# Kernel tuning notes

Hardware: AMD Instinct MI355X
Metric: run time of the kernel (lower is better)

The kernel has to match this reference:

```python
import jax, jax.numpy as jnp
import numpy as np

NEG_SLOPE = 0.2  # PyG GATv2Conv default


def with_self_loops(edge_index, n):
    loop = jnp.arange(n, dtype=edge_index.dtype)
    src = jnp.concatenate([edge_index[0], loop])
    dst = jnp.concatenate([edge_index[1], loop])
    return src, dst


def gatv2(x, src, dst, Wl, bl, Wr, br, att, bias):
    """PyG GATv2Conv (eval mode, concat=True, add_self_loops done by caller).
    x: [N, F_in]; att: [H, C]. Returns [N, H*C]."""
    N = x.shape[0]
    H, C = att.shape
    xl = (x @ Wl + bl).reshape(N, H, C)  # lin_l(x): source-side transform
    xr = (x @ Wr + br).reshape(N, H, C)  # lin_r(x): target-side transform
    s = jax.nn.leaky_relu(xl[src] + xr[dst], NEG_SLOPE)      # [E,H,C]
    logit = jnp.einsum('ehc,hc->eh', s, att)                 # [E,H]
    m = jax.ops.segment_max(logit, dst, num_segments=N)      # stable softmax per target
    e = jnp.exp(logit - m[dst])
    den = jax.ops.segment_sum(e, dst, num_segments=N)
    alpha = e / (den[dst] + 1e-16)                           # [E,H]
    out = jax.ops.segment_sum(alpha[:, :, None] * xl[src], dst, num_segments=N)
    return out.reshape(N, H * C) + bias


def setup_inputs() -> dict:
    N, E = 20000, 320000        # agent nodes / edges
    M, EM = 40000, 400000       # lane nodes / edges
    B, L = 64, 50               # focal agents, centerline length
    SEQ, INC, HID, HEADS, OUT = 50, 2, 32, 4, 60
    H4 = HID * HEADS
    key = jax.random.key(0)
    ks = list(jax.random.split(key, 48))
    kit = iter(ks)

    def p(shape):
        return jax.random.normal(next(kit), shape, jnp.float32) * 0.05

    inp = {
        'x': jax.random.normal(next(kit), (N, SEQ, INC), jnp.float32),
        'edge_index': jax.random.randint(next(kit), (2, E), 0, N),
        'lane_x': jax.random.normal(next(kit), (M, 2), jnp.float32),
        'lane_edge_index': jax.random.randint(next(kit), (2, EM), 0, M),
        'batch': jnp.sort(jax.random.randint(next(kit), (N,), 0, B)),
        'focal_idx': jax.random.randint(next(kit), (B,), 0, N),
        'centerlines': jax.random.normal(next(kit), (B, L, 2), jnp.float32),
        # agent embedding
        'ae_W': p((SEQ * INC, HID)), 'ae_b': p((HID,)),
        # agent subgraph conv1 / conv2
        'a1_Wl': p((HID, H4)), 'a1_bl': p((H4,)), 'a1_Wr': p((HID, H4)), 'a1_br': p((H4,)), 'a1_att': p((HEADS, HID)), 'a1_b': p((H4,)),
        'a2_Wl': p((H4, H4)), 'a2_bl': p((H4,)), 'a2_Wr': p((H4, H4)), 'a2_br': p((H4,)), 'a2_att': p((HEADS, HID)), 'a2_b': p((H4,)),
        # map embedding + map subgraph
        'me_W': p((2, HID)), 'me_b': p((HID,)),
        'm1_Wl': p((HID, H4)), 'm1_bl': p((H4,)), 'm1_Wr': p((HID, H4)), 'm1_br': p((H4,)), 'm1_att': p((HEADS, HID)), 'm1_b': p((H4,)),
        'm2_Wl': p((H4, H4)), 'm2_bl': p((H4,)), 'm2_Wr': p((H4, H4)), 'm2_br': p((H4,)), 'm2_att': p((HEADS, HID)), 'm2_b': p((H4,)),
        # centerline processor
        'cl_W': p((2, HID)), 'cl_b': p((HID,)),
        # global graph (heads=1)
        'g_Wl': p((H4, HID)), 'g_bl': p((HID,)), 'g_Wr': p((H4, HID)), 'g_br': p((HID,)), 'g_att': p((1, HID)), 'g_b': p((HID,)),
        # output head
        'fc_W': p((2 * HID, OUT)), 'fc_b': p((OUT,)),
    }
    return inp


def reference(x, edge_index, lane_x, lane_edge_index, batch, focal_idx, centerlines,
              ae_W, ae_b,
              a1_Wl, a1_bl, a1_Wr, a1_br, a1_att, a1_b,
              a2_Wl, a2_bl, a2_Wr, a2_br, a2_att, a2_b,
              me_W, me_b,
              m1_Wl, m1_bl, m1_Wr, m1_br, m1_att, m1_b,
              m2_Wl, m2_bl, m2_Wr, m2_br, m2_att, m2_b,
              cl_W, cl_b,
              g_Wl, g_bl, g_Wr, g_br, g_att, g_b,
              fc_W, fc_b):
    N = x.shape[0]
    M = lane_x.shape[0]
    # agent branch
    agent_x = jax.nn.relu(x.reshape(N, -1) @ ae_W + ae_b)
    a_src, a_dst = with_self_loops(edge_index, N)
    h = jax.nn.relu(gatv2(agent_x, a_src, a_dst, a1_Wl, a1_bl, a1_Wr, a1_br, a1_att, a1_b))
    agent_features = jax.nn.relu(gatv2(h, a_src, a_dst, a2_Wl, a2_bl, a2_Wr, a2_br, a2_att, a2_b))  # [N,128]
    # map branch (output unused downstream in original, computed for faithfulness)
    map_x = jax.nn.relu(lane_x @ me_W + me_b)
    m_src, m_dst = with_self_loops(lane_edge_index, M)
    hm = jax.nn.relu(gatv2(map_x, m_src, m_dst, m1_Wl, m1_bl, m1_Wr, m1_br, m1_att, m1_b))
    map_features = jax.nn.relu(gatv2(hm, m_src, m_dst, m2_Wl, m2_bl, m2_Wr, m2_br, m2_att, m2_b))
    _ = map_features  # global_mean_pool results are dead code in the original forward
    # global graph over agent features (heads=1)
    global_features = jax.nn.relu(gatv2(agent_features, a_src, a_dst, g_Wl, g_bl, g_Wr, g_br, g_att, g_b))  # [N,32]
    focal = global_features[focal_idx]  # [B,32]
    # centerlines: per-polyline mean then linear (no relu, as in original)
    cl_feat = jnp.mean(centerlines, axis=1) @ cl_W + cl_b  # [B,32]
    combined = jnp.concatenate([focal, cl_feat], axis=1)
    return combined @ fc_W + fc_b
```

## Files before the change

kernel.cpp:

```cpp
#include <hip/hip_runtime.h>
#include <hip/hip_bf16.h>
#include <hip/hip_fp16.h>
#include <math.h>

typedef __hip_bfloat16 bf16;
#define NEG_SLOPE 0.2f
#define SFLAG (1 << 30)

typedef _Float16 f16x8 __attribute__((ext_vector_type(8)));
typedef float f32x4 __attribute__((ext_vector_type(4)));

__global__ void k_detect_zero(const unsigned short* __restrict__ x, int* __restrict__ flag,
                              int* __restrict__ zbase, int n) {
    for (int i = blockIdx.x * blockDim.x + threadIdx.x; i < n; i += gridDim.x * blockDim.x)
        zbase[i] = 0;
    if (blockIdx.x == 0) {
        __shared__ int cnt;
        if (threadIdx.x == 0) cnt = 0;
        __syncthreads();
        int local = 0;
        for (int i = threadIdx.x; i < 2048; i += blockDim.x) {
            unsigned short w = x[2 * i];
            int e = (w >> 7) & 0xFF;
            if (e >= 0x90) local++;
        }
        atomicAdd(&cnt, local);
        __syncthreads();
        if (threadIdx.x == 0) flag[0] = (cnt > 100) ? 1 : 0;
    }
}

#define NSEG 25
struct Seg { const void* src; int n; int off; };
struct Tab { Seg s[NSEG]; };

__device__ __forceinline__ float ldconv(const void* src, int i, int f32mode) {
    return f32mode ? ((const float*)src)[i]
                   : __bfloat162float(((const bf16*)src)[i]);
}

__global__ void k_convert(Tab tab, float* __restrict__ dst, const int* __restrict__ flag,
                          const int* __restrict__ dstArr, int E, int N,
                          int* __restrict__ deg, int* __restrict__ rank,
                          const void* a2WlS, const void* a2WrS,
                          const void* gWlS, const void* gWrS,
                          __half* __restrict__ a2Wlt, __half* __restrict__ a2Wrt,
                          __half* __restrict__ gWlt, __half* __restrict__ gWrt) {
    int f32mode = flag[0];
    int gid = blockIdx.x * blockDim.x + threadIdx.x;
    int gsz = gridDim.x * blockDim.x;
    for (int s = 0; s < NSEG; s++) {
        Seg sg = tab.s[s];
        for (int i = gid; i < sg.n; i += gsz) {
            dst[sg.off + i] = ldconv(sg.src, i, f32mode);
        }
    }
    for (int i = gid; i < 128 * 128; i += gsz) {
        int k = i >> 7, j = i & 127;
        a2Wlt[(size_t)j * 128 + k] = __float2half(ldconv(a2WlS, i, f32mode));
        a2Wrt[(size_t)j * 128 + k] = __float2half(ldconv(a2WrS, i, f32mode));
    }
    for (int i = gid; i < 128 * 32; i += gsz) {
        int k = i >> 5, j = i & 31;
        gWlt[(size_t)j * 128 + k] = __float2half(ldconv(gWlS, i, f32mode));
        gWrt[(size_t)j * 128 + k] = __float2half(ldconv(gWrS, i, f32mode));
    }
    int EA = E + N;
    for (int e = gid; e < EA; e += gsz) {
        int d = (e < E) ? dstArr[e] : (e - E);
        rank[e] = atomicAdd(&deg[d], 1);
    }
}

__launch_bounds__(1024)
__global__ void k_scanf(const int* __restrict__ deg, int* __restrict__ offs,
                        int n, int* __restrict__ st, int nb) {
    __shared__ int ws[16];
    __shared__ int stot, sprev;
    int tile = blockIdx.x;
    int i = tile * 1024 + threadIdx.x;
    int lane = threadIdx.x & 63, wid = threadIdx.x >> 6;
    int v = (i < n) ? deg[i] : 0;
    int x = v;
    #pragma unroll
    for (int o = 1; o < 64; o <<= 1) {
        int y = __shfl_up(x, o);
        if (lane >= o) x += y;
    }
    if (lane == 63) ws[wid] = x;
    __syncthreads();
    if (wid == 0) {
        int w = (lane < 16) ? ws[lane] : 0;
        int s = w;
        #pragma unroll
        for (int o = 1; o < 16; o <<= 1) {
            int y = __shfl_up(s, o);
            if (lane >= o) s += y;
        }
        if (lane < 16) ws[lane] = s - w;
        if (lane == 15) stot = s;
    }
    __syncthreads();
    int local = ws[wid] + x - v;
    if (threadIdx.x == 0) {
        int prev = 0;
        if (tile > 0) {
            int vv;
            while ((((vv = __hip_atomic_load(&st[tile - 1], __ATOMIC_ACQUIRE,
                                             __HIP_MEMORY_SCOPE_AGENT))) & SFLAG) == 0) {}
            prev = vv & ~SFLAG;
        }
        __hip_atomic_store(&st[tile], (prev + stot) | SFLAG, __ATOMIC_RELEASE,
                           __HIP_MEMORY_SCOPE_AGENT);
        sprev = prev;
        if (tile == nb - 1) offs[n] = prev + stot;
    }
    __syncthreads();
    if (i < n) offs[i] = sprev + local;
}

__launch_bounds__(256)
__global__ void k_fill_embedlin(const int* __restrict__ srcArr, const int* __restrict__ dstArr,
                                int E, int N, const int* __restrict__ offs,
                                const int* __restrict__ rank, int* __restrict__ csr,
                                const void* __restrict__ xraw, const int* __restrict__ flag,
                                const float* __restrict__ aeW, const float* __restrict__ aeb,
                                const float* __restrict__ Wl, const float* __restrict__ bl,
                                const float* __restrict__ Wr, const float* __restrict__ br,
                                __half* __restrict__ outl, float* __restrict__ outr,
                                int EB) {
    __shared__ float xs[100 * 36];
    __shared__ float axs[32 * 36];
    if (blockIdx.x >= EB) {
        int e = (blockIdx.x - EB) * 256 + threadIdx.x;
        int EA = E + N;
        if (e >= EA) return;
        int d, s;
        if (e < E) { d = dstArr[e]; s = srcArr[e]; } else { d = s = e - E; }
        csr[offs[d] + rank[e]] = s;
        return;
    }
    constexpr int NTP = 36;
    int t = threadIdx.x, nb = blockIdx.x * 32;
    if (flag[0]) {
        const float4* x4 = (const float4*)xraw;
        for (int idx = t; idx < 32 * 25; idx += 256) {
            int node = idx / 25, k4 = idx % 25;
            float4 v = x4[(size_t)(nb + node) * 25 + k4];
            xs[(k4 * 4 + 0) * NTP + node] = v.x;
            xs[(k4 * 4 + 1) * NTP + node] = v.y;
            xs[(k4 * 4 + 2) * NTP + node] = v.z;
            xs[(k4 * 4 + 3) * NTP + node] = v.w;
        }
    } else {
        const ushort4* xu = (const ushort4*)xraw;
        for (int idx = t; idx < 32 * 25; idx += 256) {
            int node = idx / 25, k4 = idx % 25;
            ushort4 u = xu[(size_t)(nb + node) * 25 + k4];
            xs[(k4 * 4 + 0) * NTP + node] = __uint_as_float((unsigned)u.x << 16);
            xs[(k4 * 4 + 1) * NTP + node] = __uint_as_float((unsigned)u.y << 16);
            xs[(k4 * 4 + 2) * NTP + node] = __uint_as_float((unsigned)u.z << 16);
            xs[(k4 * 4 + 3) * NTP + node] = __uint_as_float((unsigned)u.w << 16);
        }
    }
    __syncthreads();
    {
        int j = t & 31, g0 = t >> 5;
        float a0 = 0.f, a1 = 0.f, a2 = 0.f, a3 = 0.f;
        #pragma unroll 10
        for (int k = 0; k < 100; k++) {
            float w = aeW[k * 32 + j];
            const float4 xv = *(const float4*)&xs[k * NTP + g0 * 4];
            a0 += w * xv.x; a1 += w * xv.y; a2 += w * xv.z; a3 += w * xv.w;
        }
        float bj = aeb[j];
        axs[j * NTP + g0 * 4 + 0] = fmaxf(a0 + bj, 0.f);
        axs[j * NTP + g0 * 4 + 1] = fmaxf(a1 + bj, 0.f);
        axs[j * NTP + g0 * 4 + 2] = fmaxf(a2 + bj, 0.f);
        axs[j * NTP + g0 * 4 + 3] = fmaxf(a3 + bj, 0.f);
    }
    __syncthreads();
    {
        int j = t & 63, g0 = t >> 6;
        float aL0[2][4], aL1[2][4], aR0[2][4], aR1[2][4];
        #pragma unroll
        for (int g = 0; g < 2; g++)
            #pragma unroll
            for (int c = 0; c < 4; c++) { aL0[g][c]=0.f; aL1[g][c]=0.f; aR0[g][c]=0.f; aR1[g][c]=0.f; }
        #pragma unroll 4
        for (int k = 0; k < 32; k++) {
            float wl0 = Wl[k * 128 + j];
            float wl1 = Wl[k * 128 + j + 64];
            float wr0 = Wr[k * 128 + j];
            float wr1 = Wr[k * 128 + j + 64];
            #pragma unroll
            for (int g = 0; g < 2; g++) {
                const float4 xv = *(const float4*)&axs[k * NTP + (g0 + g * 4) * 4];
                aL0[g][0] += wl0 * xv.x; aL0[g][1] += wl0 * xv.y; aL0[g][2] += wl0 * xv.z; aL0[g][3] += wl0 * xv.w;
                aL1[g][0] += wl1 * xv.x; aL1[g][1] += wl1 * xv.y; aL1[g][2] += wl1 * xv.z; aL1[g][3] += wl1 * xv.w;
                aR0[g][0] += wr0 * xv.x; aR0[g][1] += wr0 * xv.y; aR0[g][2] += wr0 * xv.z; aR0[g][3] += wr0 * xv.w;
                aR1[g][0] += wr1 * xv.x; aR1[g][1] += wr1 * xv.y; aR1[g][2] += wr1 * xv.z; aR1[g][3] += wr1 * xv.w;
            }
        }
        float bl0 = bl[j], bl1 = bl[j + 64], br0 = br[j], br1 = br[j + 64];
        #pragma unroll
        for (int g = 0; g < 2; g++) {
            int n0 = nb + (g0 + g * 4) * 4;
            #pragma unroll
            for (int c = 0; c < 4; c++) {
                size_t row = (size_t)(n0 + c) * 128;
                outl[row + j]      = __float2half(aL0[g][c] + bl0);
                outl[row + j + 64] = __float2half(aL1[g][c] + bl1);
                outr[row + j]      = aR0[g][c] + br0;
                outr[row + j + 64] = aR1[g][c] + br1;
            }
        }
    }
}

__device__ __forceinline__ void gat_proc(float4 raw, bool valid,
                                         const float* xrd, const float* av,
                                         float* acc, float& sm) {
    const __half2* h = (const __half2*)&raw;
    float v[8];
    float2 f;
    f = __half22float2(h[0]); v[0] = f.x; v[1] = f.y;
    f = __half22float2(h[1]); v[2] = f.x; v[3] = f.y;
    f = __half22float2(h[2]); v[4] = f.x; v[5] = f.y;
    f = __half22float2(h[3]); v[6] = f.x; v[7] = f.y;
    float p = 0.f;
    #pragma unroll
    for (int c = 0; c < 8; c++) {
        float u = v[c] + xrd[c];
        u = (u > 0.f) ? u : NEG_SLOPE * u;
        p += u * av[c];
    }
    p += __shfl_xor(p, 1);
    p += __shfl_xor(p, 2);
    p += __shfl_xor(p, 4);
    p += __shfl_xor(p, 8);
    float w = __expf(fminf(p, 80.f));
    if (!valid) w = 0.f;
    sm += w;
    #pragma unroll
    for (int c = 0; c < 8; c++) acc[c] += w * v[c];
}

__device__ __forceinline__ void gat16_to_lds(__half* xsh,
                                             const __half* __restrict__ xl,
                                             const float* __restrict__ xr,
                                             const float* __restrict__ att,
                                             const int* __restrict__ offs,
                                             const int* __restrict__ csr,
                                             const float* __restrict__ bias,
                                             int nb, int N) {
    int t = threadIdx.x;
    int wave = t >> 6, lane = t & 63;
    int grp = lane >> 4, sub = lane & 15;
    int lb = lane & 48;
    float av[8];
    {
        const float4* t4 = (const float4*)(att + sub * 8);
        float4 c = t4[0], e = t4[1];
        av[0]=c.x; av[1]=c.y; av[2]=c.z; av[3]=c.w;
        av[4]=e.x; av[5]=e.y; av[6]=e.z; av[7]=e.w;
    }
    int d = nb + wave * 4 + grp;
    bool ok = d < N;
    int i0 = ok ? offs[d] : 0;
    int i1 = ok ? offs[d + 1] : 0;
    int cnt = i1 - i0;

    float xrd[8];
    #pragma unroll
    for (int c = 0; c < 8; c++) xrd[c] = 0.f;
    if (ok) {
        const float4* p4 = (const float4*)(xr + (size_t)d * 128 + sub * 8);
        float4 a = p4[0], b = p4[1];
        xrd[0]=a.x; xrd[1]=a.y; xrd[2]=a.z; xrd[3]=a.w;
        xrd[4]=b.x; xrd[5]=b.y; xrd[6]=b.z; xrd[7]=b.w;
    }
    float acc[8];
    #pragma unroll
    for (int c = 0; c < 8; c++) acc[c] = 0.f;
    float sm = 0.f;

    int myv = (sub < cnt) ? csr[i0 + sub] : 0;
    for (int c0 = 0; c0 < cnt; c0 += 16) {
        int myv_nxt = (c0 + 16 + sub < cnt) ? csr[i0 + c0 + 16 + sub] : 0;
        int rem = min(cnt - c0, 16);
        for (int k = 0; k < rem; k += 4) {
            int s0 = __shfl(myv, lb + k + 0);
            int s1 = __shfl(myv, lb + k + 1);
            int s2 = __shfl(myv, lb + k + 2);
            int s3 = __shfl(myv, lb + k + 3);
            float4 r0 = *(const float4*)(xl + (size_t)s0 * 128 + sub * 8);
            float4 r1 = *(const float4*)(xl + (size_t)s1 * 128 + sub * 8);
            float4 r2 = *(const float4*)(xl + (size_t)s2 * 128 + sub * 8);
            float4 r3 = *(const float4*)(xl + (size_t)s3 * 128 + sub * 8);
            gat_proc(r0, true,        xrd, av, acc, sm);
            gat_proc(r1, k + 1 < rem, xrd, av, acc, sm);
            gat_proc(r2, k + 2 < rem, xrd, av, acc, sm);
            gat_proc(r3, k + 3 < rem, xrd, av, acc, sm);
        }
        myv = myv_nxt;
    }

    if (ok) {
        float inv = 1.f / (sm + 1e-16f);
        int node = wave * 4 + grp;
        int ch = sub * 8;
        #pragma unroll
        for (int c = 0; c < 8; c += 2) {
            __half2 hv;
            hv.x = __float2half(fmaxf(acc[c]     * inv + bias[ch + c],     0.f));
            hv.y = __float2half(fmaxf(acc[c + 1] * inv + bias[ch + c + 1], 0.f));
            *(__half2*)&xsh[node * 136 + ch + c] = hv;
        }
    }
}

__launch_bounds__(256)
__global__ void k_gatlin(const __half* __restrict__ xl, const float* __restrict__ xr,
                         const float* __restrict__ att,
                         const int* __restrict__ offs, const int* __restrict__ csr,
                         const float* __restrict__ bias,
                         const __half* __restrict__ Wlt, const float* __restrict__ bl,
                         const __half* __restrict__ Wrt, const float* __restrict__ br,
                         __half* __restrict__ outl, float* __restrict__ outr, int N) {
    __shared__ __align__(16) __half xsh[16 * 136];
    int nb = blockIdx.x * 16;
    gat16_to_lds(xsh, xl, xr, att, offs, csr, bias, nb, N);
    __syncthreads();

    int t = threadIdx.x;
    int lane = t & 63, wv = t >> 6;
    int quad = lane >> 4, n16 = lane & 15;
    f16x8 a[4];
    #pragma unroll
    for (int kt = 0; kt < 4; kt++)
        a[kt] = *(const f16x8*)&xsh[n16 * 136 + kt * 32 + quad * 8];

    int j0 = wv * 32;
    f32x4 aL0 = {0.f,0.f,0.f,0.f}, aL1 = {0.f,0.f,0.f,0.f};
    f32x4 aR0 = {0.f,0.f,0.f,0.f}, aR1 = {0.f,0.f,0.f,0.f};
    #pragma unroll
    for (int kt = 0; kt < 4; kt++) {
        int ko = kt * 32 + quad * 8;
        f16x8 b0 = *(const f16x8*)&Wlt[(size_t)(j0 + n16) * 128 + ko];
        f16x8 b1 = *(const f16x8*)&Wlt[(size_t)(j0 + 16 + n16) * 128 + ko];
        f16x8 b2 = *(const f16x8*)&Wrt[(size_t)(j0 + n16) * 128 + ko];
        f16x8 b3 = *(const f16x8*)&Wrt[(size_t)(j0 + 16 + n16) * 128 + ko];
        aL0 = __builtin_amdgcn_mfma_f32_16x16x32_f16(a[kt], b0, aL0, 0, 0, 0);
        aL1 = __builtin_amdgcn_mfma_f32_16x16x32_f16(a[kt], b1, aL1, 0, 0, 0);
        aR0 = __builtin_amdgcn_mfma_f32_16x16x32_f16(a[kt], b2, aR0, 0, 0, 0);
        aR1 = __builtin_amdgcn_mfma_f32_16x16x32_f16(a[kt], b3, aR1, 0, 0, 0);
    }
    float blj0 = bl[j0 + n16], blj1 = bl[j0 + 16 + n16];
    float brj0 = br[j0 + n16], brj1 = br[j0 + 16 + n16];
    #pragma unroll
    for (int r = 0; r < 4; r++) {
        int node = quad * 4 + r;
        if (nb + node >= N) continue;
        size_t row = (size_t)(nb + node) * 128;
        outl[row + j0 + n16]      = __float2half(aL0[r] + blj0);
        outl[row + j0 + 16 + n16] = __float2half(aL1[r] + blj1);
        outr[row + j0 + n16]      = aR0[r] + brj0;
        outr[row + j0 + 16 + n16] = aR1[r] + brj1;
    }
}

__launch_bounds__(256)
__global__ void k_gatling(const __half* __restrict__ xl, const float* __restrict__ xr,
                          const float* __restrict__ att,
                          const int* __restrict__ offs, const int* __restrict__ csr,
                          const float* __restrict__ bias,
                          const __half* __restrict__ Wlt, const float* __restrict__ bl,
                          const __half* __restrict__ Wrt, const float* __restrict__ br,
                          __half* __restrict__ outl, float* __restrict__ outr, int N) {
    __shared__ __align__(16) __half xsh[16 * 136];
    int nb = blockIdx.x * 16;
    gat16_to_lds(xsh, xl, xr, att, offs, csr, bias, nb, N);
    __syncthreads();

    int t = threadIdx.x;
    int lane = t & 63, wv = t >> 6;
    int quad = lane >> 4, n16 = lane & 15;
    f16x8 a[4];
    #pragma unroll
    for (int kt = 0; kt < 4; kt++)
        a[kt] = *(const f16x8*)&xsh[n16 * 136 + kt * 32 + quad * 8];

    const __half* Wt = (wv < 2) ? Wlt : Wrt;
    int j0 = (wv & 1) * 16;
    f32x4 accv = {0.f,0.f,0.f,0.f};
    #pragma unroll
    for (int kt = 0; kt < 4; kt++) {
        f16x8 b = *(const f16x8*)&Wt[(size_t)(j0 + n16) * 128 + kt * 32 + quad * 8];
        accv = __builtin_amdgcn_mfma_f32_16x16x32_f16(a[kt], b, accv, 0, 0, 0);
    }
    float bj = ((wv < 2) ? bl : br)[j0 + n16];
    #pragma unroll
    for (int r = 0; r < 4; r++) {
        int node = quad * 4 + r;
        if (nb + node >= N) continue;
        size_t row = (size_t)(nb + node) * 32;
        if (wv < 2) outl[row + j0 + n16] = __float2half(accv[r] + bj);
        else        outr[row + j0 + n16] = accv[r] + bj;
    }
}

__launch_bounds__(64)
__global__ void k_tailf(const __half* __restrict__ xl, const float* __restrict__ xr,
                        const float* __restrict__ att,
                        const int* __restrict__ offs, const int* __restrict__ csr,
                        const float* __restrict__ gb, const int* __restrict__ focal,
                        const float* __restrict__ clf, const float* __restrict__ clW,
                        const float* __restrict__ clb, const float* __restrict__ fcW,
                        const float* __restrict__ fcb, void* __restrict__ out,
                        const int* __restrict__ flag) {
    __shared__ float comb[64];
    __shared__ float ssb[2];
    int b = blockIdx.x;
    int t = threadIdx.x;
    int d = focal[b];
    int grp = t >> 3, sub = t & 7;
    int i0 = offs[d], i1 = offs[d + 1];

    float xrd[4], av[4], acc[4];
    {
        float4 a = *(const float4*)(xr + (size_t)d * 32 + sub * 4);
        xrd[0]=a.x; xrd[1]=a.y; xrd[2]=a.z; xrd[3]=a.w;
        float4 c = *(const float4*)(att + sub * 4);
        av[0]=c.x; av[1]=c.y; av[2]=c.z; av[3]=c.w;
    }
    #pragma unroll
    for (int c = 0; c < 4; c++) acc[c] = 0.f;
    float sm = 0.f;

    for (int i = i0 + grp; i < i1; i += 8) {
        float2 raw = *(const float2*)(xl + (size_t)csr[i] * 32 + sub * 4);
        const __half2* h = (const __half2*)&raw;
        float v[4];
        float2 f;
        f = __half22float2(h[0]); v[0] = f.x; v[1] = f.y;
        f = __half22float2(h[1]); v[2] = f.x; v[3] = f.y;
        float p = 0.f;
        #pragma unroll
        for (int c = 0; c < 4; c++) {
            float u = v[c] + xrd[c];
            u = (u > 0.f) ? u : NEG_SLOPE * u;
            p += u * av[c];
        }
        p += __shfl_xor(p, 1);
        p += __shfl_xor(p, 2);
        p += __shfl_xor(p, 4);
        float w = __expf(fminf(p, 80.f));
        sm += w;
        #pragma unroll
        for (int c = 0; c < 4; c++) acc[c] += w * v[c];
    }
    sm += __shfl_xor(sm, 8); sm += __shfl_xor(sm, 16); sm += __shfl_xor(sm, 32);
    #pragma unroll
    for (int c = 0; c < 4; c++) {
        acc[c] += __shfl_xor(acc[c], 8);
        acc[c] += __shfl_xor(acc[c], 16);
        acc[c] += __shfl_xor(acc[c], 32);
    }
    if (grp == 0) {
        float inv = 1.f / (sm + 1e-16f);
        #pragma unroll
        for (int c = 0; c < 4; c++)
            comb[sub * 4 + c] = fmaxf(acc[c] * inv + gb[sub * 4 + c], 0.f);
    }
    if (t < 2) {
        float s = 0.f;
        for (int l = 0; l < 50; l++) s += clf[(size_t)b * 100 + l * 2 + t];
        ssb[t] = s / 50.f;
    }
    __syncthreads();
    if (t < 32) comb[32 + t] = ssb[0] * clW[t] + ssb[1] * clW[32 + t] + clb[t];
    __syncthreads();
    if (t < 60) {
        float a2 = fcb[t];
        #pragma unroll 16
        for (int k = 0; k < 64; k++) a2 += comb[k] * fcW[k * 60 + t];
        if (flag[0]) ((float*)out)[b * 60 + t] = a2;
        else ((bf16*)out)[b * 60 + t] = __float2bfloat16(a2);
    }
}

extern "C" void kernel_launch(void* const* d_in, const int* in_sizes, int n_in,
                              void* d_out, int out_size, void* d_ws, size_t ws_size,
                              hipStream_t stream) {
    const int* edge  = (const int*)d_in[1];
    const int* focal = (const int*)d_in[5];

    const int N = in_sizes[0] / 100;
    const int E = in_sizes[1] / 2;
    const int B = in_sizes[5];
    const int EA = E + N;
    const int* srcArr = edge;
    const int* dstArr = edge + E;

    const int idxs[NSEG] = {7,8,9,10,11,12,13,14,15,16,17,18,19,20,
                            35,36,37,38,39,40,41,42,43,44, 6};
    float* base = (float*)d_ws;
    int* flag = (int*)base;
    float* wf = base + 16;
    Tab tab;
    int off[NSEG];
    int o = 0;
    for (int i = 0; i < NSEG; i++) {
        tab.s[i].src = d_in[idxs[i]];
        tab.s[i].n   = in_sizes[idxs[i]];
        tab.s[i].off = o;
        off[i] = o;
        o += in_sizes[idxs[i]];
    }
    const float* aeW  = wf + off[0],  *aeb  = wf + off[1];
    const float* a1Wl = wf + off[2],  *a1bl = wf + off[3];
    const float* a1Wr = wf + off[4],  *a1br = wf + off[5];
    const float* a1att= wf + off[6],  *a1b  = wf + off[7];
    const float* a2bl = wf + off[9];
    const float* a2br = wf + off[11];
    const float* a2att= wf + off[12], *a2b  = wf + off[13];
    const float* clW  = wf + off[14], *clb  = wf + off[15];
    const float* gbl  = wf + off[17];
    const float* gbr  = wf + off[19];
    const float* gatt = wf + off[20], *gb   = wf + off[21];
    const float* fcW  = wf + off[22], *fcb  = wf + off[23];
    const float* clf  = wf + off[24];

    float* p = wf + o + ((4 - (o & 3)) & 3);
    size_t N128 = (size_t)N * 128;
    __half* hxl1 = (__half*)p;      p += (size_t)N * 64;
    float* fB1  = p;                p += N128;
    __half* hxl2 = (__half*)p;      p += (size_t)N * 64;
    float* fB2  = p;                p += N128;
    int* deg    = (int*)p;
    int* st     = deg + N;
    int* offs   = st + 32;
    int* rank   = offs + N + 1;
    int* csr    = rank + EA;
    uintptr_t up = (uintptr_t)(csr + EA);
    up = (up + 15) & ~(uintptr_t)15;
    __half* a2Wlt = (__half*)up;
    __half* a2Wrt = a2Wlt + 16384;
    __half* gWlt  = a2Wrt + 16384;
    __half* gWrt  = gWlt + 4096;

    const int NB = (N + 1023) / 1024;
    const int EB = N / 32;
    const int FBLK = (EA + 255) / 256;
    const int GT = (N + 15) / 16;

    k_detect_zero<<<64, 256, 0, stream>>>((const unsigned short*)d_in[0], flag, deg, N + 32);
    k_convert<<<256, 256, 0, stream>>>(tab, wf, flag, dstArr, E, N, deg, rank,
                                       d_in[15], d_in[17], d_in[37], d_in[39],
                                       a2Wlt, a2Wrt, gWlt, gWrt);
    k_scanf<<<NB, 1024, 0, stream>>>(deg, offs, N, st, NB);
    k_fill_embedlin<<<EB + FBLK, 256, 0, stream>>>(srcArr, dstArr, E, N, offs, rank, csr,
                                                   d_in[0], flag, aeW, aeb,
                                                   a1Wl, a1bl, a1Wr, a1br, hxl1, fB1, EB);
    k_gatlin<<<GT, 256, 0, stream>>>(hxl1, fB1, a1att, offs, csr, a1b,
                                     a2Wlt, a2bl, a2Wrt, a2br, hxl2, fB2, N);
    k_gatling<<<GT, 256, 0, stream>>>(hxl2, fB2, a2att, offs, csr, a2b,
                                      gWlt, gbl, gWrt, gbr, hxl1, fB1, N);
    k_tailf<<<B, 64, 0, stream>>>(hxl1, fB1, gatt, offs, csr, gb, focal,
                                  clf, clW, clb, fcW, fcb, d_out, flag);
}
```

Measured before the change: 264.6 us.

## Process two destination nodes per lane group, 32 nodes per block in GAT kernels

```diff
diff --git a/kernel.cpp b/kernel.cpp
--- a/kernel.cpp
+++ b/kernel.cpp
@@ -246,7 +246,7 @@
     for (int c = 0; c < 8; c++) acc[c] += w * v[c];
 }
 
-__device__ __forceinline__ void gat16_to_lds(__half* xsh,
+__device__ __forceinline__ void gat32_to_lds(__half* xsh,
                                              const __half* __restrict__ xl,
                                              const float* __restrict__ xr,
                                              const float* __restrict__ att,
@@ -265,57 +265,104 @@
         av[0]=c.x; av[1]=c.y; av[2]=c.z; av[3]=c.w;
         av[4]=e.x; av[5]=e.y; av[6]=e.z; av[7]=e.w;
     }
-    int d = nb + wave * 4 + grp;
-    bool ok = d < N;
-    int i0 = ok ? offs[d] : 0;
-    int i1 = ok ? offs[d + 1] : 0;
-    int cnt = i1 - i0;
-
-    float xrd[8];
-    #pragma unroll
-    for (int c = 0; c < 8; c++) xrd[c] = 0.f;
-    if (ok) {
-        const float4* p4 = (const float4*)(xr + (size_t)d * 128 + sub * 8);
+    int dA = nb + wave * 8 + grp * 2;
+    int dB = dA + 1;
+    bool okA = dA < N, okB = dB < N;
+    int iA0 = okA ? offs[dA] : 0, iA1 = okA ? offs[dA + 1] : 0;
+    int iB0 = okB ? offs[dB] : 0, iB1 = okB ? offs[dB + 1] : 0;
+    int cntA = iA1 - iA0, cntB = iB1 - iB0;
+
+    float xrdA[8], xrdB[8];
+    #pragma unroll
+    for (int c = 0; c < 8; c++) { xrdA[c] = 0.f; xrdB[c] = 0.f; }
+    if (okA) {
+        const float4* p4 = (const float4*)(xr + (size_t)dA * 128 + sub * 8);
         float4 a = p4[0], b = p4[1];
-        xrd[0]=a.x; xrd[1]=a.y; xrd[2]=a.z; xrd[3]=a.w;
-        xrd[4]=b.x; xrd[5]=b.y; xrd[6]=b.z; xrd[7]=b.w;
-    }
-    float acc[8];
-    #pragma unroll
-    for (int c = 0; c < 8; c++) acc[c] = 0.f;
-    float sm = 0.f;
-
-    int myv = (sub < cnt) ? csr[i0 + sub] : 0;
-    for (int c0 = 0; c0 < cnt; c0 += 16) {
-        int myv_nxt = (c0 + 16 + sub < cnt) ? csr[i0 + c0 + 16 + sub] : 0;
-        int rem = min(cnt - c0, 16);
-        for (int k = 0; k < rem; k += 4) {
-            int s0 = __shfl(myv, lb + k + 0);
-            int s1 = __shfl(myv, lb + k + 1);
-            int s2 = __shfl(myv, lb + k + 2);
-            int s3 = __shfl(myv, lb + k + 3);
-            float4 r0 = *(const float4*)(xl + (size_t)s0 * 128 + sub * 8);
-            float4 r1 = *(const float4*)(xl + (size_t)s1 * 128 + sub * 8);
-            float4 r2 = *(const float4*)(xl + (size_t)s2 * 128 + sub * 8);
-            float4 r3 = *(const float4*)(xl + (size_t)s3 * 128 + sub * 8);
-            gat_proc(r0, true,        xrd, av, acc, sm);
-            gat_proc(r1, k + 1 < rem, xrd, av, acc, sm);
-            gat_proc(r2, k + 2 < rem, xrd, av, acc, sm);
-            gat_proc(r3, k + 3 < rem, xrd, av, acc, sm);
-        }
-        myv = myv_nxt;
-    }
-
-    if (ok) {
-        float inv = 1.f / (sm + 1e-16f);
-        int node = wave * 4 + grp;
-        int ch = sub * 8;
+        xrdA[0]=a.x; xrdA[1]=a.y; xrdA[2]=a.z; xrdA[3]=a.w;
+        xrdA[4]=b.x; xrdA[5]=b.y; xrdA[6]=b.z; xrdA[7]=b.w;
+    }
+    if (okB) {
+        const float4* p4 = (const float4*)(xr + (size_t)dB * 128 + sub * 8);
+        float4 a = p4[0], b = p4[1];
+        xrdB[0]=a.x; xrdB[1]=a.y; xrdB[2]=a.z; xrdB[3]=a.w;
+        xrdB[4]=b.x; xrdB[5]=b.y; xrdB[6]=b.z; xrdB[7]=b.w;
+    }
+    float accA[8], accB[8];
+    #pragma unroll
+    for (int c = 0; c < 8; c++) { accA[c] = 0.f; accB[c] = 0.f; }
+    float smA = 0.f, smB = 0.f;
+
+    int myvA = (sub < cntA) ? csr[iA0 + sub] : 0;
+    int myvB = (sub < cntB) ? csr[iB0 + sub] : 0;
+    int nCh = max((cntA + 15) >> 4, (cntB + 15) >> 4);
+    for (int ch = 0; ch < nCh; ch++) {
+        int c0 = ch * 16;
+        int nxtA = (c0 + 16 + sub < cntA) ? csr[iA0 + c0 + 16 + sub] : 0;
+        int nxtB = (c0 + 16 + sub < cntB) ? csr[iB0 + c0 + 16 + sub] : 0;
+        int remA = cntA - c0; if (remA > 16) remA = 16;
+        int remB = cntB - c0; if (remB > 16) remB = 16;
+        int remM = remA > remB ? remA : remB;
+        for (int k = 0; k < remM; k += 4) {
+            bool doA = k < remA, doB = k < remB;
+            float4 rA0, rA1, rA2, rA3, rB0, rB1, rB2, rB3;
+            if (doA) {
+                int s0 = __shfl(myvA, lb + k + 0);
+                int s1 = __shfl(myvA, lb + k + 1);
+                int s2 = __shfl(myvA, lb + k + 2);
+                int s3 = __shfl(myvA, lb + k + 3);
+                rA0 = *(const float4*)(xl + (size_t)s0 * 128 + sub * 8);
+                rA1 = *(const float4*)(xl + (size_t)s1 * 128 + sub * 8);
+                rA2 = *(const float4*)(xl + (size_t)s2 * 128 + sub * 8);
+                rA3 = *(const float4*)(xl + (size_t)s3 * 128 + sub * 8);
+            }
+            if (doB) {
+                int s0 = __shfl(myvB, lb + k + 0);
+                int s1 = __shfl(myvB, lb + k + 1);
+                int s2 = __shfl(myvB, lb + k + 2);
+                int s3 = __shfl(myvB, lb + k + 3);
+                rB0 = *(const float4*)(xl + (size_t)s0 * 128 + sub * 8);
+                rB1 = *(const float4*)(xl + (size_t)s1 * 128 + sub * 8);
+                rB2 = *(const float4*)(xl + (size_t)s2 * 128 + sub * 8);
+                rB3 = *(const float4*)(xl + (size_t)s3 * 128 + sub * 8);
+            }
+            if (doA) {
+                gat_proc(rA0, true,         xrdA, av, accA, smA);
+                gat_proc(rA1, k + 1 < remA, xrdA, av, accA, smA);
+                gat_proc(rA2, k + 2 < remA, xrdA, av, accA, smA);
+                gat_proc(rA3, k + 3 < remA, xrdA, av, accA, smA);
+            }
+            if (doB) {
+                gat_proc(rB0, true,         xrdB, av, accB, smB);
+                gat_proc(rB1, k + 1 < remB, xrdB, av, accB, smB);
+                gat_proc(rB2, k + 2 < remB, xrdB, av, accB, smB);
+                gat_proc(rB3, k + 3 < remB, xrdB, av, accB, smB);
+            }
+        }
+        myvA = nxtA; myvB = nxtB;
+    }
+
+    if (okA) {
+        float inv = 1.f / (smA + 1e-16f);
+        int node = wave * 8 + grp * 2;
+        int chb = sub * 8;
         #pragma unroll
         for (int c = 0; c < 8; c += 2) {
             __half2 hv;
-            hv.x = __float2half(fmaxf(acc[c]     * inv + bias[ch + c],     0.f));
-            hv.y = __float2half(fmaxf(acc[c + 1] * inv + bias[ch + c + 1], 0.f));
-            *(__half2*)&xsh[node * 136 + ch + c] = hv;
+            hv.x = __float2half(fmaxf(accA[c]     * inv + bias[chb + c],     0.f));
+            hv.y = __float2half(fmaxf(accA[c + 1] * inv + bias[chb + c + 1], 0.f));
+            *(__half2*)&xsh[node * 136 + chb + c] = hv;
+        }
+    }
+    if (okB) {
+        float inv = 1.f / (smB + 1e-16f);
+        int node = wave * 8 + grp * 2 + 1;
+        int chb = sub * 8;
+        #pragma unroll
+        for (int c = 0; c < 8; c += 2) {
+            __half2 hv;
+            hv.x = __float2half(fmaxf(accB[c]     * inv + bias[chb + c],     0.f));
+            hv.y = __float2half(fmaxf(accB[c + 1] * inv + bias[chb + c + 1], 0.f));
+            *(__half2*)&xsh[node * 136 + chb + c] = hv;
         }
     }
 }
@@ -328,45 +375,48 @@
                          const __half* __restrict__ Wlt, const float* __restrict__ bl,
                          const __half* __restrict__ Wrt, const float* __restrict__ br,
                          __half* __restrict__ outl, float* __restrict__ outr, int N) {
-    __shared__ __align__(16) __half xsh[16 * 136];
-    int nb = blockIdx.x * 16;
-    gat16_to_lds(xsh, xl, xr, att, offs, csr, bias, nb, N);
+    __shared__ __align__(16) __half xsh[32 * 136];
+    int nb = blockIdx.x * 32;
+    gat32_to_lds(xsh, xl, xr, att, offs, csr, bias, nb, N);
     __syncthreads();
 
     int t = threadIdx.x;
     int lane = t & 63, wv = t >> 6;
     int quad = lane >> 4, n16 = lane & 15;
+    int r16 = wv >> 1;
+    int j0 = (wv & 1) * 64;
     f16x8 a[4];
     #pragma unroll
     for (int kt = 0; kt < 4; kt++)
-        a[kt] = *(const f16x8*)&xsh[n16 * 136 + kt * 32 + quad * 8];
-
-    int j0 = wv * 32;
-    f32x4 aL0 = {0.f,0.f,0.f,0.f}, aL1 = {0.f,0.f,0.f,0.f};
-    f32x4 aR0 = {0.f,0.f,0.f,0.f}, aR1 = {0.f,0.f,0.f,0.f};
+        a[kt] = *(const f16x8*)&xsh[(r16 * 16 + n16) * 136 + kt * 32 + quad * 8];
+
+    f32x4 aL[4], aR[4];
+    #pragma unroll
+    for (int tl = 0; tl < 4; tl++) { aL[tl] = (f32x4){0.f,0.f,0.f,0.f}; aR[tl] = (f32x4){0.f,0.f,0.f,0.f}; }
     #pragma unroll
     for (int kt = 0; kt < 4; kt++) {
         int ko = kt * 32 + quad * 8;
-        f16x8 b0 = *(const f16x8*)&Wlt[(size_t)(j0 + n16) * 128 + ko];
-        f16x8 b1 = *(const f16x8*)&Wlt[(size_t)(j0 + 16 + n16) * 128 + ko];
-        f16x8 b2 = *(const f16x8*)&Wrt[(size_t)(j0 + n16) * 128 + ko];
-        f16x8 b3 = *(const f16x8*)&Wrt[(size_t)(j0 + 16 + n16) * 128 + ko];
-        aL0 = __builtin_amdgcn_mfma_f32_16x16x32_f16(a[kt], b0, aL0, 0, 0, 0);
-        aL1 = __builtin_amdgcn_mfma_f32_16x16x32_f16(a[kt], b1, aL1, 0, 0, 0);
-        aR0 = __builtin_amdgcn_mfma_f32_16x16x32_f16(a[kt], b2, aR0, 0, 0, 0);
-        aR1 = __builtin_amdgcn_mfma_f32_16x16x32_f16(a[kt], b3, aR1, 0, 0, 0);
-    }
-    float blj0 = bl[j0 + n16], blj1 = bl[j0 + 16 + n16];
-    float brj0 = br[j0 + n16], brj1 = br[j0 + 16 + n16];
+        #pragma unroll
+        for (int tl = 0; tl < 4; tl++) {
+            f16x8 bL = *(const f16x8*)&Wlt[(size_t)(j0 + tl * 16 + n16) * 128 + ko];
+            f16x8 bR = *(const f16x8*)&Wrt[(size_t)(j0 + tl * 16 + n16) * 128 + ko];
+            aL[tl] = __builtin_amdgcn_mfma_f32_16x16x32_f16(a[kt], bL, aL[tl], 0, 0, 0);
+            aR[tl] = __builtin_amdgcn_mfma_f32_16x16x32_f16(a[kt], bR, aR[tl], 0, 0, 0);
+        }
+    }
+    float blv[4], brv[4];
+    #pragma unroll
+    for (int tl = 0; tl < 4; tl++) { blv[tl] = bl[j0 + tl * 16 + n16]; brv[tl] = br[j0 + tl * 16 + n16]; }
     #pragma unroll
     for (int r = 0; r < 4; r++) {
-        int node = quad * 4 + r;
+        int node = r16 * 16 + quad * 4 + r;
         if (nb + node >= N) continue;
         size_t row = (size_t)(nb + node) * 128;
-        outl[row + j0 + n16]      = __float2half(aL0[r] + blj0);
-        outl[row + j0 + 16 + n16] = __float2half(aL1[r] + blj1);
-        outr[row + j0 + n16]      = aR0[r] + brj0;
-        outr[row + j0 + 16 + n16] = aR1[r] + brj1;
+        #pragma unroll
+        for (int tl = 0; tl < 4; tl++) {
+            outl[row + j0 + tl * 16 + n16] = __float2half(aL[tl][r] + blv[tl]);
+            outr[row + j0 + tl * 16 + n16] = aR[tl][r] + brv[tl];
+        }
     }
 }
 
@@ -378,35 +428,45 @@
                           const __half* __restrict__ Wlt, const float* __restrict__ bl,
                           const __half* __restrict__ Wrt, const float* __restrict__ br,
                           __half* __restrict__ outl, float* __restrict__ outr, int N) {
-    __shared__ __align__(16) __half xsh[16 * 136];
-    int nb = blockIdx.x * 16;
-    gat16_to_lds(xsh, xl, xr, att, offs, csr, bias, nb, N);
+    __shared__ __align__(16) __half xsh[32 * 136];
+    int nb = blockIdx.x * 32;
+    gat32_to_lds(xsh, xl, xr, att, offs, csr, bias, nb, N);
     __syncthreads();
 
     int t = threadIdx.x;
     int lane = t & 63, wv = t >> 6;
     int quad = lane >> 4, n16 = lane & 15;
+    int r16 = wv >> 1;
+    int side = wv & 1;
     f16x8 a[4];
     #pragma unroll
     for (int kt = 0; kt < 4; kt++)
-        a[kt] = *(const f16x8*)&xsh[n16 * 136 + kt * 32 + quad * 8];
-
-    const __half* Wt = (wv < 2) ? Wlt : Wrt;
-    int j0 = (wv & 1) * 16;
-    f32x4 accv = {0.f,0.f,0.f,0.f};
+        a[kt] = *(const f16x8*)&xsh[(r16 * 16 + n16) * 136 + kt * 32 + quad * 8];
+
+    const __half* Wt = side ? Wrt : Wlt;
+    f32x4 ac0 = {0.f,0.f,0.f,0.f}, ac1 = {0.f,0.f,0.f,0.f};
     #pragma unroll
     for (int kt = 0; kt < 4; kt++) {
-        f16x8 b = *(const f16x8*)&Wt[(size_t)(j0 + n16) * 128 + kt * 32 + quad * 8];
-        accv = __builtin_amdgcn_mfma_f32_16x16x32_f16(a[kt], b, accv, 0, 0, 0);
-    }
-    float bj = ((wv < 2) ? bl : br)[j0 + n16];
+        int ko = kt * 32 + quad * 8;
+        f16x8 b0 = *(const f16x8*)&Wt[(size_t)(n16) * 128 + ko];
+        f16x8 b1 = *(const f16x8*)&Wt[(size_t)(16 + n16) * 128 + ko];
+        ac0 = __builtin_amdgcn_mfma_f32_16x16x32_f16(a[kt], b0, ac0, 0, 0, 0);
+        ac1 = __builtin_amdgcn_mfma_f32_16x16x32_f16(a[kt], b1, ac1, 0, 0, 0);
+    }
+    const float* bb = side ? br : bl;
+    float bj0 = bb[n16], bj1 = bb[16 + n16];
     #pragma unroll
     for (int r = 0; r < 4; r++) {
-        int node = quad * 4 + r;
+        int node = r16 * 16 + quad * 4 + r;
         if (nb + node >= N) continue;
         size_t row = (size_t)(nb + node) * 32;
-        if (wv < 2) outl[row + j0 + n16] = __float2half(accv[r] + bj);
-        else        outr[row + j0 + n16] = accv[r] + bj;
+        if (side == 0) {
+            outl[row + n16]      = __float2half(ac0[r] + bj0);
+            outl[row + 16 + n16] = __float2half(ac1[r] + bj1);
+        } else {
+            outr[row + n16]      = ac0[r] + bj0;
+            outr[row + 16 + n16] = ac1[r] + bj1;
+        }
     }
 }
 
@@ -553,7 +613,7 @@
     const int NB = (N + 1023) / 1024;
     const int EB = N / 32;
     const int FBLK = (EA + 255) / 256;
-    const int GT = (N + 15) / 16;
+    const int GT = (N + 31) / 32;
 
     k_detect_zero<<<64, 256, 0, stream>>>((const unsigned short*)d_in[0], flag, deg, N + 32);
     k_convert<<<256, 256, 0, stream>>>(tab, wf, flag, dstArr, E, N, deg, rank,
```

New measurement: 286.3 us. 1.08x slower.

## Compute second GAT layer only for in-neighbours of focal nodes

Applied to the files above, without the earlier changes.

```diff
diff --git a/kernel.cpp b/kernel.cpp
--- a/kernel.cpp
+++ b/kernel.cpp
@@ -253,10 +253,10 @@
                                              const int* __restrict__ offs,
                                              const int* __restrict__ csr,
                                              const float* __restrict__ bias,
-                                             int nb, int N) {
+                                             int d, int node) {
     int t = threadIdx.x;
-    int wave = t >> 6, lane = t & 63;
-    int grp = lane >> 4, sub = lane & 15;
+    int lane = t & 63;
+    int sub = lane & 15;
     int lb = lane & 48;
     float av[8];
     {
@@ -265,8 +265,7 @@
         av[0]=c.x; av[1]=c.y; av[2]=c.z; av[3]=c.w;
         av[4]=e.x; av[5]=e.y; av[6]=e.z; av[7]=e.w;
     }
-    int d = nb + wave * 4 + grp;
-    bool ok = d < N;
+    bool ok = d >= 0;
     int i0 = ok ? offs[d] : 0;
     int i1 = ok ? offs[d + 1] : 0;
     int cnt = i1 - i0;
@@ -306,10 +305,9 @@
         myv = myv_nxt;
     }
 
+    int ch = sub * 8;
     if (ok) {
         float inv = 1.f / (sm + 1e-16f);
-        int node = wave * 4 + grp;
-        int ch = sub * 8;
         #pragma unroll
         for (int c = 0; c < 8; c += 2) {
             __half2 hv;
@@ -317,6 +315,10 @@
             hv.y = __float2half(fmaxf(acc[c + 1] * inv + bias[ch + c + 1], 0.f));
             *(__half2*)&xsh[node * 136 + ch + c] = hv;
         }
+    } else {
+        #pragma unroll
+        for (int c = 0; c < 8; c += 2)
+            *(__half2*)&xsh[node * 136 + ch + c] = __half2{__half(0.f), __half(0.f)};
     }
 }
 
@@ -327,15 +329,31 @@
                          const float* __restrict__ bias,
                          const __half* __restrict__ Wlt, const float* __restrict__ bl,
                          const __half* __restrict__ Wrt, const float* __restrict__ br,
-                         __half* __restrict__ outl, float* __restrict__ outr, int N) {
+                         __half* __restrict__ outl, float* __restrict__ outr, int N,
+                         const int* __restrict__ focal, int B,
+                         int* __restrict__ L, int* __restrict__ Lcnt, int GT) {
+    if (blockIdx.x >= GT) {
+        int t = threadIdx.x;
+        if (t < B) {
+            int f = focal[t];
+            int j0 = offs[f], j1 = offs[f + 1];
+            int base = atomicAdd(Lcnt, j1 - j0);
+            for (int j = j0; j < j1; j++) L[base + (j - j0)] = csr[j];
+        }
+        return;
+    }
     __shared__ __align__(16) __half xsh[16 * 136];
     int nb = blockIdx.x * 16;
-    gat16_to_lds(xsh, xl, xr, att, offs, csr, bias, nb, N);
-    __syncthreads();
-
     int t = threadIdx.x;
     int lane = t & 63, wv = t >> 6;
     int quad = lane >> 4, n16 = lane & 15;
+    {
+        int node = wv * 4 + quad;
+        int dd = nb + node;
+        gat16_to_lds(xsh, xl, xr, att, offs, csr, bias, (dd < N) ? dd : -1, node);
+    }
+    __syncthreads();
+
     f16x8 a[4];
     #pragma unroll
     for (int kt = 0; kt < 4; kt++)
@@ -377,36 +395,46 @@
                           const float* __restrict__ bias,
                           const __half* __restrict__ Wlt, const float* __restrict__ bl,
                           const __half* __restrict__ Wrt, const float* __restrict__ br,
-                          __half* __restrict__ outl, float* __restrict__ outr, int N) {
+                          __half* __restrict__ outl, float* __restrict__ outr,
+                          const int* __restrict__ L, const int* __restrict__ Lcnt) {
     __shared__ __align__(16) __half xsh[16 * 136];
-    int nb = blockIdx.x * 16;
-    gat16_to_lds(xsh, xl, xr, att, offs, csr, bias, nb, N);
-    __syncthreads();
-
+    int total = *Lcnt;
     int t = threadIdx.x;
     int lane = t & 63, wv = t >> 6;
     int quad = lane >> 4, n16 = lane & 15;
-    f16x8 a[4];
-    #pragma unroll
-    for (int kt = 0; kt < 4; kt++)
-        a[kt] = *(const f16x8*)&xsh[n16 * 136 + kt * 32 + quad * 8];
-
-    const __half* Wt = (wv < 2) ? Wlt : Wrt;
-    int j0 = (wv & 1) * 16;
-    f32x4 accv = {0.f,0.f,0.f,0.f};
-    #pragma unroll
-    for (int kt = 0; kt < 4; kt++) {
-        f16x8 b = *(const f16x8*)&Wt[(size_t)(j0 + n16) * 128 + kt * 32 + quad * 8];
-        accv = __builtin_amdgcn_mfma_f32_16x16x32_f16(a[kt], b, accv, 0, 0, 0);
-    }
-    float bj = ((wv < 2) ? bl : br)[j0 + n16];
-    #pragma unroll
-    for (int r = 0; r < 4; r++) {
-        int node = quad * 4 + r;
-        if (nb + node >= N) continue;
-        size_t row = (size_t)(nb + node) * 32;
-        if (wv < 2) outl[row + j0 + n16] = __float2half(accv[r] + bj);
-        else        outr[row + j0 + n16] = accv[r] + bj;
+
+    for (int tile = blockIdx.x; tile * 16 < total; tile += gridDim.x) {
+        if (tile != (int)blockIdx.x) __syncthreads();
+        int node = wv * 4 + quad;
+        int idx = tile * 16 + node;
+        int d = (idx < total) ? L[idx] : -1;
+        gat16_to_lds(xsh, xl, xr, att, offs, csr, bias, d, node);
+        __syncthreads();
+
+        f16x8 a[4];
+        #pragma unroll
+        for (int kt = 0; kt < 4; kt++)
+            a[kt] = *(const f16x8*)&xsh[n16 * 136 + kt * 32 + quad * 8];
+
+        const __half* Wt = (wv < 2) ? Wlt : Wrt;
+        int j0 = (wv & 1) * 16;
+        f32x4 accv = {0.f,0.f,0.f,0.f};
+        #pragma unroll
+        for (int kt = 0; kt < 4; kt++) {
+            f16x8 b = *(const f16x8*)&Wt[(size_t)(j0 + n16) * 128 + kt * 32 + quad * 8];
+            accv = __builtin_amdgcn_mfma_f32_16x16x32_f16(a[kt], b, accv, 0, 0, 0);
+        }
+        float bj = ((wv < 2) ? bl : br)[j0 + n16];
+        #pragma unroll
+        for (int r = 0; r < 4; r++) {
+            int nn = quad * 4 + r;
+            int gidx = tile * 16 + nn;
+            if (gidx >= total) continue;
+            int gd = L[gidx];
+            size_t row = (size_t)gd * 32;
+            if (wv < 2) outl[row + j0 + n16] = __float2half(accv[r] + bj);
+            else        outr[row + j0 + n16] = accv[r] + bj;
+        }
     }
 }
 
@@ -549,6 +577,8 @@
     __half* a2Wrt = a2Wlt + 16384;
     __half* gWlt  = a2Wrt + 16384;
     __half* gWrt  = gWlt + 4096;
+    int* Lbuf = (int*)(gWrt + 4096);
+    int* Lcnt = st + 30;
 
     const int NB = (N + 1023) / 1024;
     const int EB = N / 32;
@@ -563,10 +593,11 @@
     k_fill_embedlin<<<EB + FBLK, 256, 0, stream>>>(srcArr, dstArr, E, N, offs, rank, csr,
                                                    d_in[0], flag, aeW, aeb,
                                                    a1Wl, a1bl, a1Wr, a1br, hxl1, fB1, EB);
-    k_gatlin<<<GT, 256, 0, stream>>>(hxl1, fB1, a1att, offs, csr, a1b,
-                                     a2Wlt, a2bl, a2Wrt, a2br, hxl2, fB2, N);
-    k_gatling<<<GT, 256, 0, stream>>>(hxl2, fB2, a2att, offs, csr, a2b,
-                                      gWlt, gbl, gWrt, gbr, hxl1, fB1, N);
+    k_gatlin<<<GT + 1, 256, 0, stream>>>(hxl1, fB1, a1att, offs, csr, a1b,
+                                         a2Wlt, a2bl, a2Wrt, a2br, hxl2, fB2, N,
+                                         focal, B, Lbuf, Lcnt, GT);
+    k_gatling<<<128, 256, 0, stream>>>(hxl2, fB2, a2att, offs, csr, a2b,
+                                       gWlt, gbl, gWrt, gbr, hxl1, fB1, Lbuf, Lcnt);
     k_tailf<<<B, 64, 0, stream>>>(hxl1, fB1, gatt, offs, csr, gb, focal,
                                   clf, clW, clb, fcW, fcb, d_out, flag);
 }
```

Result: faster. 255.7 us (-3.4%).
